# Kernel tuning notes

Hardware: AMD Instinct MI355X
Metric: run time of the kernel (lower is better)

The kernel has to match this reference:

```python
import jax, jax.numpy as jnp
import numpy as np

D = 100  # input_size


def _gru_scan(x, h0, wi, wh, bi, bh):
    # x: [B,T,Din], h0: [B,H], wi: [3H,Din], wh: [3H,H]  (PyTorch r,z,n gate order)
    xw = jnp.einsum('btd,gd->btg', x, wi) + bi  # [B,T,3H]
    def step(h, xt):
        gh = h @ wh.T + bh
        xr, xz, xn = jnp.split(xt, 3, axis=-1)
        hr, hz, hn = jnp.split(gh, 3, axis=-1)
        r = jax.nn.sigmoid(xr + hr)
        z = jax.nn.sigmoid(xz + hz)
        n = jnp.tanh(xn + r * hn)
        hn2 = (1 - z) * n + z * h
        return hn2, hn2
    _, ys = jax.lax.scan(step, h0, jnp.swapaxes(xw, 0, 1))
    return jnp.swapaxes(ys, 0, 1)  # [B,T,H]


def _bigru(x, wi, wh, bi, bh):
    B = x.shape[0]
    H = wh.shape[-1]
    h0 = jnp.zeros((B, H), x.dtype)
    f = _gru_scan(x, h0, wi[0], wh[0], bi[0], bh[0])
    b = _gru_scan(x[:, ::-1], h0, wi[1], wh[1], bi[1], bh[1])[:, ::-1]
    return jnp.concatenate([f, b], axis=-1)


def _gru_cell(x, h, wi, wh, bi, bh):
    gx = x @ wi.T + bi
    gh = h @ wh.T + bh
    xr, xz, xn = jnp.split(gx, 3, axis=-1)
    hr, hz, hn = jnp.split(gh, 3, axis=-1)
    r = jax.nn.sigmoid(xr + hr)
    z = jax.nn.sigmoid(xz + hz)
    n = jnp.tanh(xn + r * hn)
    return (1 - z) * n + z * h


def setup_inputs() -> dict:
    key = jax.random.key(0)
    ks = iter(jax.random.split(key, 40))
    def n(shape, s=0.08):
        return (jax.random.normal(next(ks), shape) * s).astype(jnp.float32)
    B, T, L, V = 32, 512, 64, 400000
    inp = {
        'x_word': jax.random.randint(next(ks), (B, T), 0, V),
        'x_query': jax.random.randint(next(ks), (B, L), 0, V),
        'embed': n((V, D), 0.3),
        'ctx_wi': n((2, 3 * D, D)), 'ctx_wh': n((2, 3 * D, D)),
        'ctx_bi': n((2, 3 * D)), 'ctx_bh': n((2, 3 * D)),
        'mod0_wi': n((2, 3 * D, 8 * D)), 'mod0_wh': n((2, 3 * D, D)),
        'mod0_bi': n((2, 3 * D)), 'mod0_bh': n((2, 3 * D)),
        'mod1_wi': n((2, 3 * D, 2 * D)), 'mod1_wh': n((2, 3 * D, D)),
        'mod1_bi': n((2, 3 * D)), 'mod1_bh': n((2, 3 * D)),
        'w_sim': n((6 * D,)),
        'enc_wi': n((12 * D, 2 * D)), 'enc_wh': n((12 * D, 4 * D)),
        'enc_bi': n((12 * D,)), 'enc_bh': n((12 * D,)),
        'dec_wi': n((12 * D, 2 * D)), 'dec_wh': n((12 * D, 4 * D)),
        'dec_bi': n((12 * D,)), 'dec_bh': n((12 * D,)),
        'w1': n((2 * D, 4 * D)), 'w2': n((2 * D, 4 * D)), 'vt': n((2 * D,)),
    }
    return inp


def reference(x_word, x_query, embed, ctx_wi, ctx_wh, ctx_bi, ctx_bh,
              mod0_wi, mod0_wh, mod0_bi, mod0_bh, mod1_wi, mod1_wh, mod1_bi, mod1_bh,
              w_sim, enc_wi, enc_wh, enc_bi, enc_bh, dec_wi, dec_wh, dec_bi, dec_bh,
              w1, w2, vt):
    B, T = x_word.shape
    # shared bidirectional context encoder over both context and query
    h = _bigru(embed[x_word], ctx_wi, ctx_wh, ctx_bi, ctx_bh)   # [B,T,2D]
    u = _bigru(embed[x_query], ctx_wi, ctx_wh, ctx_bi, ctx_bh)  # [B,L,2D]
    # trilinear similarity W @ cat(h,u,h*u), fused (no [B,T,L,6D] materialization)
    w1s, w2s, w3s = jnp.split(w_sim, 3)
    S = (jnp.einsum('btd,d->bt', h, w1s)[:, :, None]
         + jnp.einsum('bld,d->bl', u, w2s)[:, None, :]
         + jnp.einsum('btd,bld->btl', h * w3s, u))               # [B,T,L]
    c2q = jnp.einsum('btl,bld->btd', jax.nn.softmax(S, axis=-1), u)
    b_att = jax.nn.softmax(jnp.max(S, axis=2), axis=-1)          # [B,T]
    q2c = jnp.einsum('bt,btd->bd', b_att, h)[:, None, :]         # [B,1,2D]
    G = jnp.concatenate([h, c2q, h * c2q, h * q2c], axis=-1)     # [B,T,8D]
    # 2-layer bidirectional modeling GRU
    M = _bigru(G, mod0_wi, mod0_wh, mod0_bi, mod0_bh)
    M = _bigru(M, mod1_wi, mod1_wh, mod1_bi, mod1_bh)            # [B,T,2D]
    # pointer network
    enc = _gru_scan(M, jnp.zeros((B, 4 * D), M.dtype), enc_wi, enc_wh, enc_bi, enc_bh)  # [B,T,4D]
    enc_w1 = jnp.einsum('bth,ph->btp', enc, w1)                  # precompute W1 @ enc
    hid = jnp.zeros((B, 4 * D), M.dtype)
    dec_in = jnp.zeros((B, 2 * D), M.dtype)  # never updated (as in original)
    probs = []
    for _ in range(2):  # answers = 2 (start, end)
        hid = _gru_cell(dec_in, hid, dec_wi, dec_wh, dec_bi, dec_bh)
        blend = jnp.tanh(enc_w1 + (hid @ w2.T)[:, None, :])      # [B,T,2D]
        out = jnp.einsum('btp,p->bt', blend, vt)
        probs.append(jax.nn.log_softmax(out, axis=-1))
    return jnp.stack(probs, axis=1)  # [B,2,T]
```

## Files before the change

kernel.cpp:

```cpp
#include <hip/hip_runtime.h>
#include <hip/hip_bf16.h>

typedef __hip_bfloat16 bf16;
typedef unsigned long long u64;
typedef __attribute__((ext_vector_type(8))) short s8v;
typedef __attribute__((ext_vector_type(4))) short s4v;
typedef __attribute__((ext_vector_type(4))) float f4v;

#define DEV __device__ __forceinline__

DEV float to_f32(float x) { return x; }
DEV float to_f32(bf16 x) { return __bfloat162float(x); }
DEV void store_c(float* p, float v) { *p = v; }
DEV void store_c(bf16* p, float v) { *p = __float2bfloat16(v); }
DEV float sigmf(float x) { return 1.f / (1.f + __expf(-x)); }

__global__ void gather_embed_bf(const int* __restrict__ idx, const float* __restrict__ embed,
                                bf16* __restrict__ out, int ntok) {
  int i = blockIdx.x * blockDim.x + threadIdx.x;
  if (i >= ntok * 100) return;
  int t = i / 100;
  int d = i - t * 100;
  out[i] = __float2bfloat16(embed[(size_t)idx[t] * 100 + d]);
}

__global__ void cvt_bf16(const float* __restrict__ in, bf16* __restrict__ out, int n) {
  int i = blockIdx.x * blockDim.x + threadIdx.x;
  if (i < n) out[i] = __float2bfloat16(in[i]);
}

template <typename TC, bool HAS_BIAS>
__global__ __launch_bounds__(256) void gemm_mfma(
    const bf16* __restrict__ A, const bf16* __restrict__ W,
    const float* __restrict__ bias, TC* __restrict__ C,
    int M, int N, int K) {
  __shared__ short Als[128 * 32];
  __shared__ short Wls[64 * 32];
  const int tid = threadIdx.x;
  const int m0 = blockIdx.x * 128;
  const int n0 = blockIdx.y * 64;
  const int lane = tid & 63;
  const int wv = tid >> 6;
  const int wm = wv >> 1, wn = wv & 1;
  const int lq = lane >> 4, lr = lane & 15;
  const int arow = tid >> 1;
  const int ah = tid & 1;
  const int wrow = (tid & 127) >> 1;

  f4v acc[4][2];
#pragma unroll
  for (int i = 0; i < 4; ++i)
#pragma unroll
    for (int j = 0; j < 2; ++j) acc[i][j] = (f4v){0.f, 0.f, 0.f, 0.f};

  for (int k0 = 0; k0 < K; k0 += 32) {
#pragma unroll
    for (int ss = 0; ss < 2; ++ss) {
      int s = 2 * ah + ss;
      int kk = k0 + s * 8;
      short* dst = &Als[arow * 32 + s * 8];
      const short* src = (const short*)(A + (size_t)(m0 + arow) * K + kk);
      if (kk + 8 <= K) {
        *(s4v*)dst = *(const s4v*)src;
        *(s4v*)(dst + 4) = *(const s4v*)(src + 4);
      } else {
#pragma unroll
        for (int j = 0; j < 8; ++j) dst[j] = (kk + j < K) ? src[j] : (short)0;
      }
    }
    if (tid < 128) {
      int nrow = n0 + wrow;
#pragma unroll
      for (int ss = 0; ss < 2; ++ss) {
        int s = 2 * (tid & 1) + ss;
        int kk = k0 + s * 8;
        short* dst = &Wls[wrow * 32 + s * 8];
        if (nrow < N) {
          const short* src = (const short*)(W + (size_t)nrow * K + kk);
          if (kk + 8 <= K) {
            *(s4v*)dst = *(const s4v*)src;
            *(s4v*)(dst + 4) = *(const s4v*)(src + 4);
          } else {
#pragma unroll
            for (int j = 0; j < 8; ++j) dst[j] = (kk + j < K) ? src[j] : (short)0;
          }
        } else {
#pragma unroll
          for (int j = 0; j < 8; ++j) dst[j] = (short)0;
        }
      }
    }
    __syncthreads();
    s8v af[4], bfr[2];
#pragma unroll
    for (int mi = 0; mi < 4; ++mi) {
      int r = wm * 64 + mi * 16 + lr;
      af[mi] = *(const s8v*)&Als[r * 32 + lq * 8];
    }
#pragma unroll
    for (int ni = 0; ni < 2; ++ni) {
      int r = wn * 32 + ni * 16 + lr;
      bfr[ni] = *(const s8v*)&Wls[r * 32 + lq * 8];
    }
#pragma unroll
    for (int mi = 0; mi < 4; ++mi)
#pragma unroll
      for (int ni = 0; ni < 2; ++ni)
        acc[mi][ni] = __builtin_amdgcn_mfma_f32_16x16x32_bf16(af[mi], bfr[ni], acc[mi][ni], 0, 0, 0);
    __syncthreads();
  }
#pragma unroll
  for (int mi = 0; mi < 4; ++mi) {
#pragma unroll
    for (int ni = 0; ni < 2; ++ni) {
      int n = n0 + wn * 32 + ni * 16 + lr;
      if (n >= N) continue;
      float bv = HAS_BIAS ? bias[n] : 0.f;
#pragma unroll
      for (int r = 0; r < 4; ++r) {
        int m = m0 + wm * 64 + mi * 16 + lq * 4 + r;
        store_c(&C[(size_t)m * N + n], acc[mi][ni][r] + bv);
      }
    }
  }
}

template <typename TO>
__global__ __launch_bounds__(320) void gru_scan100_reg(
    const bf16* __restrict__ xw_f, const bf16* __restrict__ xw_b,
    const float* __restrict__ wh,
    const float* __restrict__ bh,
    TO* __restrict__ out,
    int T) {
  const int b = blockIdx.x, dir = blockIdx.y;
  const bf16* xw = dir ? xw_b : xw_f;
  __shared__ float h_s[100];
  __shared__ float g_s[300];
  const int tid = threadIdx.x;
  float w[100];
  float bias = 0.f;
  if (tid < 300) {
    const float* wrow = wh + (size_t)dir * 30000 + (size_t)tid * 100;
#pragma unroll
    for (int c = 0; c < 25; ++c) {
      float4 v = *(const float4*)(wrow + 4 * c);
      w[4 * c] = v.x; w[4 * c + 1] = v.y; w[4 * c + 2] = v.z; w[4 * c + 3] = v.w;
    }
    bias = bh[dir * 300 + tid];
  }
  if (tid < 100) h_s[tid] = 0.f;
  __syncthreads();
  for (int step = 0; step < T; ++step) {
    int t = dir ? (T - 1 - step) : step;
    if (tid < 300) {
      float a0 = bias, a1 = 0.f, a2 = 0.f, a3 = 0.f;
#pragma unroll
      for (int c = 0; c < 25; ++c) {
        float4 h4 = *(const float4*)(&h_s[4 * c]);
        a0 += w[4 * c] * h4.x; a1 += w[4 * c + 1] * h4.y;
        a2 += w[4 * c + 2] * h4.z; a3 += w[4 * c + 3] * h4.w;
      }
      g_s[tid] = (a0 + a1) + (a2 + a3);
    }
    __syncthreads();
    if (tid < 100) {
      size_t base = ((size_t)b * T + t) * 300;
      float xr = to_f32(xw[base + tid]);
      float xz = to_f32(xw[base + 100 + tid]);
      float xn = to_f32(xw[base + 200 + tid]);
      float rr = sigmf(xr + g_s[tid]);
      float zz = sigmf(xz + g_s[100 + tid]);
      float nn = tanhf(xn + rr * g_s[200 + tid]);
      float hn = (1.f - zz) * nn + zz * h_s[tid];
      h_s[tid] = hn;
      store_c(&out[((size_t)b * T + t) * 200 + dir * 100 + tid], hn);
    }
    __syncthreads();
  }
}

__global__ __launch_bounds__(640) void gru_scan_enc_tag(
    const bf16* __restrict__ xw,
    const float* __restrict__ wh,
    const float* __restrict__ bh,
    bf16* __restrict__ out,
    u64* __restrict__ hx,
    int T) {
  const int b = blockIdx.x, s = blockIdx.y;
  __shared__ float h_s[400];
  __shared__ float g_s[150];
  const int tid = threadIdx.x;
  const int g = tid >> 2, p = tid & 3;
  const bool active = (tid < 600);
  float w[100];
  float bias = 0.f;
  if (active) {
    int i = g % 50, grp = g / 50;
    int gidx = grp * 400 + s * 50 + i;
    const float* wrow = wh + (size_t)gidx * 400 + p * 100;
#pragma unroll
    for (int c = 0; c < 25; ++c) {
      float4 v = *(const float4*)(wrow + 4 * c);
      w[4 * c] = v.x; w[4 * c + 1] = v.y; w[4 * c + 2] = v.z; w[4 * c + 3] = v.w;
    }
    if (p == 0) bias = bh[gidx];
  }
  for (int k = tid; k < 400; k += 640) h_s[k] = 0.f;
  const int myi = s * 50 + tid;
  float pxr = 0.f, pxz = 0.f, pxn = 0.f;
  if (tid < 50) {
    size_t base0 = (size_t)b * T * 1200;
    pxr = to_f32(xw[base0 + myi]);
    pxz = to_f32(xw[base0 + 400 + myi]);
    pxn = to_f32(xw[base0 + 800 + myi]);
  }
  __syncthreads();

  for (int t = 0; t < T; ++t) {
    if (active) {
      float a0 = bias, a1 = 0.f, a2 = 0.f, a3 = 0.f;
      const int hb = p * 100;
#pragma unroll
      for (int c = 0; c < 25; ++c) {
        float4 h4 = *(const float4*)(&h_s[hb + 4 * c]);
        a0 += w[4 * c] * h4.x; a1 += w[4 * c + 1] * h4.y;
        a2 += w[4 * c + 2] * h4.z; a3 += w[4 * c + 3] * h4.w;
      }
      float acc = (a0 + a1) + (a2 + a3);
      acc += __shfl_xor(acc, 1);
      acc += __shfl_xor(acc, 2);
      if (p == 0) g_s[g] = acc;
    }
    __syncthreads();
    const int par = (t + 1) & 1;
    u64* hxp = hx + ((size_t)b * 2 + par) * 400;
    if (tid < 50) {
      float rr = sigmf(pxr + g_s[tid]);
      float zz = sigmf(pxz + g_s[50 + tid]);
      float nn = tanhf(pxn + rr * g_s[100 + tid]);
      float hn = (1.f - zz) * nn + zz * h_s[myi];
      out[((size_t)b * T + t) * 400 + myi] = __float2bfloat16(hn);
      h_s[myi] = hn;
      u64 pack = (u64)__float_as_uint(hn) | ((u64)(unsigned)(t + 1) << 32);
      __hip_atomic_store(&hxp[myi], pack, __ATOMIC_RELAXED, __HIP_MEMORY_SCOPE_AGENT);
      if (t + 1 < T) {
        size_t basen = ((size_t)b * T + (t + 1)) * 1200;
        pxr = to_f32(xw[basen + myi]);
        pxz = to_f32(xw[basen + 400 + myi]);
        pxn = to_f32(xw[basen + 800 + myi]);
      }
    }
    if (tid < 400 && (tid / 50) != s) {
      const u64* src = &hxp[tid];
      u64 v;
      for (;;) {
        v = __hip_atomic_load(src, __ATOMIC_RELAXED, __HIP_MEMORY_SCOPE_AGENT);
        if ((unsigned)(v >> 32) == (unsigned)(t + 1)) break;
        __builtin_amdgcn_s_sleep(1);
      }
      h_s[tid] = __uint_as_float((unsigned)v);
    }
    __syncthreads();
  }
}

__global__ __launch_bounds__(64) void rowdot200(const float* __restrict__ X, const float* __restrict__ w,
                                                float* __restrict__ out, int rows) {
  int r = blockIdx.x;
  int lane = threadIdx.x;
  const float* x = X + (size_t)r * 200;
  float s = x[lane] * w[lane] + x[lane + 64] * w[lane + 64] + x[lane + 128] * w[lane + 128];
  if (lane < 8) s += x[lane + 192] * w[lane + 192];
  for (int off = 32; off; off >>= 1) s += __shfl_down(s, off);
  if (lane == 0) out[r] = s;
}

__global__ __launch_bounds__(256) void attn_main(
    const float* __restrict__ h,
    const float* __restrict__ u,
    const float* __restrict__ th,
    const float* __restrict__ tu,
    const float* __restrict__ w_sim,
    float* __restrict__ c2q,
    float* __restrict__ smax,
    int T) {
  const int b = blockIdx.x;
  const int t0 = blockIdx.y * 32;
  __shared__ float u_s[64 * 201];
  __shared__ float tu_s[64];
  __shared__ float w3_s[200];
  __shared__ float hw3_s[200];
  __shared__ float Sp[4][64];
  __shared__ float A_s[64];
  const int tid = threadIdx.x;
  for (int i = tid; i < 64 * 200; i += 256) {
    int l = i / 200, d = i - l * 200;
    u_s[l * 201 + d] = u[((size_t)b * 64 + l) * 200 + d];
  }
  if (tid < 64) tu_s[tid] = tu[b * 64 + tid];
  if (tid < 200) w3_s[tid] = w_sim[400 + tid];
  __syncthreads();
  for (int tt = 0; tt < 32; ++tt) {
    int t = t0 + tt;
    if (tid < 200) hw3_s[tid] = h[((size_t)b * T + t) * 200 + tid] * w3_s[tid];
    __syncthreads();
    int l = tid & 63, q = tid >> 6;
    float p = 0.f;
    for (int d = q * 50; d < q * 50 + 50; ++d) p += hw3_s[d] * u_s[l * 201 + d];
    Sp[q][l] = p;
    __syncthreads();
    if (tid < 64) {
      float s = th[b * T + t] + tu_s[l] + Sp[0][l] + Sp[1][l] + Sp[2][l] + Sp[3][l];
      float m = s;
      for (int off = 32; off; off >>= 1) m = fmaxf(m, __shfl_xor(m, off));
      float e = __expf(s - m);
      float ssum = e;
      for (int off = 32; off; off >>= 1) ssum += __shfl_xor(ssum, off);
      A_s[l] = e / ssum;
      if (l == 0) smax[b * T + t] = m;
    }
    __syncthreads();
    if (tid < 200) {
      float acc = 0.f;
      for (int l2 = 0; l2 < 64; ++l2) acc += A_s[l2] * u_s[l2 * 201 + tid];
      c2q[((size_t)b * T + t) * 200 + tid] = acc;
    }
    __syncthreads();
  }
}

__global__ __launch_bounds__(256) void softmax_T(const float* __restrict__ in, float* __restrict__ outv, int T) {
  int b = blockIdx.x;
  int tid = threadIdx.x;
  __shared__ float red[256];
  float m = -1e30f;
  for (int t = tid; t < T; t += 256) m = fmaxf(m, in[b * T + t]);
  red[tid] = m;
  __syncthreads();
  for (int s = 128; s; s >>= 1) {
    if (tid < s) red[tid] = fmaxf(red[tid], red[tid + s]);
    __syncthreads();
  }
  m = red[0];
  __syncthreads();
  float sum = 0.f;
  for (int t = tid; t < T; t += 256) sum += __expf(in[b * T + t] - m);
  red[tid] = sum;
  __syncthreads();
  for (int s = 128; s; s >>= 1) {
    if (tid < s) red[tid] += red[tid + s];
    __syncthreads();
  }
  float inv = 1.f / red[0];
  for (int t = tid; t < T; t += 256) outv[b * T + t] = __expf(in[b * T + t] - m) * inv;
}

__global__ __launch_bounds__(256) void q2c_kernel(const float* __restrict__ batt, const float* __restrict__ h,
                                                  float* __restrict__ q2c, int T) {
  int b = blockIdx.x;
  int tid = threadIdx.x;
  if (tid < 200) {
    float acc = 0.f;
    for (int t = 0; t < T; ++t) acc += batt[b * T + t] * h[((size_t)b * T + t) * 200 + tid];
    q2c[b * 200 + tid] = acc;
  }
}

__global__ void build_G(const float* __restrict__ h, const float* __restrict__ c2q,
                        const float* __restrict__ q2c, bf16* __restrict__ G, int T) {
  size_t i = (size_t)blockIdx.x * blockDim.x + threadIdx.x;
  if (i >= (size_t)32 * T * 200) return;
  size_t row = i / 200;
  int d = (int)(i - row * 200);
  int b = (int)(row / T);
  float hv = h[i];
  float cv = c2q[i];
  float qv = q2c[b * 200 + d];
  bf16* g = G + row * 800;
  g[d] = __float2bfloat16(hv);
  g[200 + d] = __float2bfloat16(cv);
  g[400 + d] = __float2bfloat16(hv * cv);
  g[600 + d] = __float2bfloat16(hv * qv);
}

__global__ __launch_bounds__(512) void decoder_small(
    const float* __restrict__ dwh,
    const float* __restrict__ dbi, const float* __restrict__ dbh,
    const float* __restrict__ w2,
    float* __restrict__ d2out) {
  __shared__ float hid[400];
  __shared__ float hid2[400];
  __shared__ float gh[1200];
  const int tid = threadIdx.x;
  if (tid < 400) {
    float r = sigmf(dbi[tid] + dbh[tid]);
    float z = sigmf(dbi[400 + tid] + dbh[400 + tid]);
    float n = tanhf(dbi[800 + tid] + r * dbh[800 + tid]);
    hid[tid] = (1.f - z) * n;
  }
  __syncthreads();
  if (tid < 200) {
    float a = 0.f;
    for (int k = 0; k < 400; ++k) a += w2[(size_t)tid * 400 + k] * hid[k];
    d2out[tid] = a;
  }
  for (int j = tid; j < 1200; j += 512) {
    float a = dbh[j];
    for (int k = 0; k < 400; ++k) a += dwh[(size_t)j * 400 + k] * hid[k];
    gh[j] = a;
  }
  __syncthreads();
  if (tid < 400) {
    float r = sigmf(dbi[tid] + gh[tid]);
    float z = sigmf(dbi[400 + tid] + gh[400 + tid]);
    float n = tanhf(dbi[800 + tid] + r * gh[800 + tid]);
    hid2[tid] = (1.f - z) * n + z * hid[tid];
  }
  __syncthreads();
  if (tid < 200) {
    float a = 0.f;
    for (int k = 0; k < 400; ++k) a += w2[(size_t)tid * 400 + k] * hid2[k];
    d2out[200 + tid] = a;
  }
}

__global__ __launch_bounds__(64) void logits_kernel(
    const float* __restrict__ encw1,
    const float* __restrict__ d2,
    const float* __restrict__ vt,
    float* __restrict__ outp,
    int T) {
  int row = blockIdx.x;
  int b = row / T, t = row - b * T;
  int lane = threadIdx.x;
  const float* e = encw1 + (size_t)row * 200;
  float s0 = 0.f, s1 = 0.f;
  for (int p = lane; p < 200; p += 64) {
    float ev = e[p], v = vt[p];
    s0 += tanhf(ev + d2[p]) * v;
    s1 += tanhf(ev + d2[200 + p]) * v;
  }
  for (int off = 32; off; off >>= 1) {
    s0 += __shfl_down(s0, off);
    s1 += __shfl_down(s1, off);
  }
  if (lane == 0) {
    outp[((size_t)b * 2 + 0) * T + t] = s0;
    outp[((size_t)b * 2 + 1) * T + t] = s1;
  }
}

__global__ __launch_bounds__(256) void log_softmax_T(float* __restrict__ x, int T) {
  int row = blockIdx.x;
  float* p = x + (size_t)row * T;
  __shared__ float red[256];
  int tid = threadIdx.x;
  float m = -1e30f;
  for (int t = tid; t < T; t += 256) m = fmaxf(m, p[t]);
  red[tid] = m;
  __syncthreads();
  for (int s = 128; s; s >>= 1) {
    if (tid < s) red[tid] = fmaxf(red[tid], red[tid + s]);
    __syncthreads();
  }
  m = red[0];
  __syncthreads();
  float sum = 0.f;
  for (int t = tid; t < T; t += 256) sum += __expf(p[t] - m);
  red[tid] = sum;
  __syncthreads();
  for (int s = 128; s; s >>= 1) {
    if (tid < s) red[tid] += red[tid + s];
    __syncthreads();
  }
  float lse = m + __logf(red[0]);
  __syncthreads();
  for (int t = tid; t < T; t += 256) p[t] = p[t] - lse;
}

extern "C" void kernel_launch(void* const* d_in, const int* in_sizes, int n_in,
                              void* d_out, int out_size, void* d_ws, size_t ws_size,
                              hipStream_t stream) {
  (void)in_sizes; (void)n_in; (void)out_size; (void)ws_size;
  const int B = 32, T = 512, L = 64;
  const int BT = B * T;
  const int BL = B * L;

  const int* x_word = (const int*)d_in[0];
  const int* x_query = (const int*)d_in[1];
  const float* embed = (const float*)d_in[2];
  const float* ctx_wi = (const float*)d_in[3];
  const float* ctx_wh = (const float*)d_in[4];
  const float* ctx_bi = (const float*)d_in[5];
  const float* ctx_bh = (const float*)d_in[6];
  const float* mod0_wi = (const float*)d_in[7];
  const float* mod0_wh = (const float*)d_in[8];
  const float* mod0_bi = (const float*)d_in[9];
  const float* mod0_bh = (const float*)d_in[10];
  const float* mod1_wi = (const float*)d_in[11];
  const float* mod1_wh = (const float*)d_in[12];
  const float* mod1_bi = (const float*)d_in[13];
  const float* mod1_bh = (const float*)d_in[14];
  const float* w_sim = (const float*)d_in[15];
  const float* enc_wi = (const float*)d_in[16];
  const float* enc_wh = (const float*)d_in[17];
  const float* enc_bi = (const float*)d_in[18];
  const float* enc_bh = (const float*)d_in[19];
  const float* dec_wh = (const float*)d_in[21];
  const float* dec_bi = (const float*)d_in[22];
  const float* dec_bh = (const float*)d_in[23];
  const float* w1 = (const float*)d_in[24];
  const float* w2 = (const float*)d_in[25];
  const float* vt = (const float*)d_in[26];
  float* out_f = (float*)d_out;

  char* ws = (char*)d_ws;
  size_t off = 0;
  auto alloc = [&](size_t bytes) -> void* {
    void* p = ws + off;
    off += (bytes + 255) & ~(size_t)255;
    return p;
  };
  u64* hx = (u64*)alloc((size_t)B * 2 * 400 * 8);
  bf16* ewbf = (bf16*)alloc((size_t)BT * 100 * 2);
  bf16* eqbf = (bf16*)alloc((size_t)BL * 100 * 2);
  bf16* ctx_wibf = (bf16*)alloc((size_t)60000 * 2);
  bf16* mod0_wibf = (bf16*)alloc((size_t)480000 * 2);
  bf16* mod1_wibf = (bf16*)alloc((size_t)120000 * 2);
  bf16* enc_wibf = (bf16*)alloc((size_t)240000 * 2);
  bf16* w1bf = (bf16*)alloc((size_t)80000 * 2);
  char* RA = (char*)alloc((size_t)BT * 1200 * 2);
  bf16* xwA = (bf16*)RA;
  bf16* xwB = (bf16*)(RA + (size_t)BT * 300 * 2);
  bf16* xwe = (bf16*)RA;
  bf16* xwqF = (bf16*)alloc((size_t)BL * 300 * 2);
  bf16* xwqB = (bf16*)alloc((size_t)BL * 300 * 2);
  char* RB = (char*)alloc((size_t)BT * 800 * 2);
  bf16* G = (bf16*)RB;
  bf16* enc_outbf = (bf16*)RB;
  char* RC = (char*)alloc((size_t)2 * BT * 200 * 4);
  float* h_cat = (float*)RC;
  float* c2q = (float*)(RC + (size_t)BT * 200 * 4);
  bf16* M0bf = (bf16*)c2q;
  bf16* Mxbf = (bf16*)h_cat;
  float* encw1 = c2q;
  float* u_cat = (float*)alloc((size_t)BL * 200 * 4);
  float* th = (float*)alloc((size_t)BT * 4);
  float* tu = (float*)alloc((size_t)BL * 4);
  float* smaxb = (float*)alloc((size_t)BT * 4);
  float* batt = (float*)alloc((size_t)BT * 4);
  float* q2cb = (float*)alloc((size_t)B * 200 * 4);
  float* d2 = (float*)alloc((size_t)400 * 4);

  hipMemsetAsync(hx, 0, (size_t)B * 2 * 400 * 8, stream);

  cvt_bf16<<<(60000 + 255) / 256, 256, 0, stream>>>(ctx_wi, ctx_wibf, 60000);
  cvt_bf16<<<(480000 + 255) / 256, 256, 0, stream>>>(mod0_wi, mod0_wibf, 480000);
  cvt_bf16<<<(120000 + 255) / 256, 256, 0, stream>>>(mod1_wi, mod1_wibf, 120000);
  cvt_bf16<<<(240000 + 255) / 256, 256, 0, stream>>>(enc_wi, enc_wibf, 240000);
  cvt_bf16<<<(80000 + 255) / 256, 256, 0, stream>>>(w1, w1bf, 80000);
  gather_embed_bf<<<(BT * 100 + 255) / 256, 256, 0, stream>>>(x_word, embed, ewbf, BT);
  gather_embed_bf<<<(BL * 100 + 255) / 256, 256, 0, stream>>>(x_query, embed, eqbf, BL);

  {
    dim3 g(BT / 128, (300 + 63) / 64);
    gemm_mfma<bf16, true><<<g, 256, 0, stream>>>(ewbf, ctx_wibf, ctx_bi, xwA, BT, 300, 100);
    gemm_mfma<bf16, true><<<g, 256, 0, stream>>>(ewbf, ctx_wibf + 30000, ctx_bi + 300, xwB, BT, 300, 100);
    dim3 gq(BL / 128, (300 + 63) / 64);
    gemm_mfma<bf16, true><<<gq, 256, 0, stream>>>(eqbf, ctx_wibf, ctx_bi, xwqF, BL, 300, 100);
    gemm_mfma<bf16, true><<<gq, 256, 0, stream>>>(eqbf, ctx_wibf + 30000, ctx_bi + 300, xwqB, BL, 300, 100);
  }

  gru_scan100_reg<float><<<dim3(B, 2), 320, 0, stream>>>(xwA, xwB, ctx_wh, ctx_bh, h_cat, T);
  gru_scan100_reg<float><<<dim3(B, 2), 320, 0, stream>>>(xwqF, xwqB, ctx_wh, ctx_bh, u_cat, L);

  rowdot200<<<BT, 64, 0, stream>>>(h_cat, w_sim, th, BT);
  rowdot200<<<BL, 64, 0, stream>>>(u_cat, w_sim + 200, tu, BL);
  attn_main<<<dim3(B, T / 32), 256, 0, stream>>>(h_cat, u_cat, th, tu, w_sim, c2q, smaxb, T);
  softmax_T<<<B, 256, 0, stream>>>(smaxb, batt, T);
  q2c_kernel<<<B, 256, 0, stream>>>(batt, h_cat, q2cb, T);
  build_G<<<(BT * 200 + 255) / 256, 256, 0, stream>>>(h_cat, c2q, q2cb, G, T);

  {
    dim3 g(BT / 128, (300 + 63) / 64);
    gemm_mfma<bf16, true><<<g, 256, 0, stream>>>(G, mod0_wibf, mod0_bi, xwA, BT, 300, 800);
    gemm_mfma<bf16, true><<<g, 256, 0, stream>>>(G, mod0_wibf + 240000, mod0_bi + 300, xwB, BT, 300, 800);
  }
  gru_scan100_reg<bf16><<<dim3(B, 2), 320, 0, stream>>>(xwA, xwB, mod0_wh, mod0_bh, M0bf, T);

  {
    dim3 g(BT / 128, (300 + 63) / 64);
    gemm_mfma<bf16, true><<<g, 256, 0, stream>>>(M0bf, mod1_wibf, mod1_bi, xwA, BT, 300, 200);
    gemm_mfma<bf16, true><<<g, 256, 0, stream>>>(M0bf, mod1_wibf + 60000, mod1_bi + 300, xwB, BT, 300, 200);
  }
  gru_scan100_reg<bf16><<<dim3(B, 2), 320, 0, stream>>>(xwA, xwB, mod1_wh, mod1_bh, Mxbf, T);

  {
    dim3 g(BT / 128, (1200 + 63) / 64);
    gemm_mfma<bf16, true><<<g, 256, 0, stream>>>(Mxbf, enc_wibf, enc_bi, xwe, BT, 1200, 200);
  }
  gru_scan_enc_tag<<<dim3(B, 8), 640, 0, stream>>>(xwe, enc_wh, enc_bh, enc_outbf, hx, T);
  {
    dim3 g(BT / 128, (200 + 63) / 64);
    gemm_mfma<float, false><<<g, 256, 0, stream>>>(enc_outbf, w1bf, nullptr, encw1, BT, 200, 400);
  }

  decoder_small<<<1, 512, 0, stream>>>(dec_wh, dec_bi, dec_bh, w2, d2);
  logits_kernel<<<BT, 64, 0, stream>>>(encw1, d2, vt, out_f, T);
  log_softmax_T<<<B * 2, 256, 0, stream>>>(out_f, T);
}
```

Measured before the change: 3.580 ms.

## Process two batch rows per encoder GRU block and prefetch gate inputs

The encoder GRU scan now handles two batch elements per block, reusing the register-resident recurrent weights for both hidden states. This halves the number of blocks and cross-block spin-waits while doubling work per step, so weight loads and sync overhead are amortized. Separately, the 100-wide bidirectional scan now prefetches the next timestep's input-gate values into registers during the current step, taking the global load latency off the serial critical path. The trade-off is a longer per-step critical path in the encoder, since each step runs two matvecs and two spin-waits in sequence, and fewer blocks to spread across the CUs.

```diff
diff --git a/kernel.cpp b/kernel.cpp
--- a/kernel.cpp
+++ b/kernel.cpp
@@ -149,6 +149,14 @@
     bias = bh[dir * 300 + tid];
   }
   if (tid < 100) h_s[tid] = 0.f;
+  float pxr = 0.f, pxz = 0.f, pxn = 0.f;
+  if (tid < 100) {
+    int t0 = dir ? (T - 1) : 0;
+    size_t base = ((size_t)b * T + t0) * 300;
+    pxr = to_f32(xw[base + tid]);
+    pxz = to_f32(xw[base + 100 + tid]);
+    pxn = to_f32(xw[base + 200 + tid]);
+  }
   __syncthreads();
   for (int step = 0; step < T; ++step) {
     int t = dir ? (T - 1 - step) : step;
@@ -164,31 +172,35 @@
     }
     __syncthreads();
     if (tid < 100) {
-      size_t base = ((size_t)b * T + t) * 300;
-      float xr = to_f32(xw[base + tid]);
-      float xz = to_f32(xw[base + 100 + tid]);
-      float xn = to_f32(xw[base + 200 + tid]);
-      float rr = sigmf(xr + g_s[tid]);
-      float zz = sigmf(xz + g_s[100 + tid]);
-      float nn = tanhf(xn + rr * g_s[200 + tid]);
+      float rr = sigmf(pxr + g_s[tid]);
+      float zz = sigmf(pxz + g_s[100 + tid]);
+      float nn = tanhf(pxn + rr * g_s[200 + tid]);
       float hn = (1.f - zz) * nn + zz * h_s[tid];
       h_s[tid] = hn;
       store_c(&out[((size_t)b * T + t) * 200 + dir * 100 + tid], hn);
-    }
-    __syncthreads();
-  }
-}
-
-__global__ __launch_bounds__(640) void gru_scan_enc_tag(
+      if (step + 1 < T) {
+        int tn = dir ? (T - 2 - step) : (step + 1);
+        size_t basen = ((size_t)b * T + tn) * 300;
+        pxr = to_f32(xw[basen + tid]);
+        pxz = to_f32(xw[basen + 100 + tid]);
+        pxn = to_f32(xw[basen + 200 + tid]);
+      }
+    }
+    __syncthreads();
+  }
+}
+
+__global__ __launch_bounds__(640) void gru_scan_enc_tag2(
     const bf16* __restrict__ xw,
     const float* __restrict__ wh,
     const float* __restrict__ bh,
     bf16* __restrict__ out,
     u64* __restrict__ hx,
     int T) {
-  const int b = blockIdx.x, s = blockIdx.y;
-  __shared__ float h_s[400];
-  __shared__ float g_s[150];
+  const int pair = blockIdx.x, s = blockIdx.y;
+  const int bA = 2 * pair, bB = 2 * pair + 1;
+  __shared__ float hA[400], hB[400];
+  __shared__ float gA[150], gB[150];
   const int tid = threadIdx.x;
   const int g = tid >> 2, p = tid & 3;
   const bool active = (tid < 600);
@@ -205,60 +217,95 @@
     }
     if (p == 0) bias = bh[gidx];
   }
-  for (int k = tid; k < 400; k += 640) h_s[k] = 0.f;
+  for (int k = tid; k < 400; k += 640) { hA[k] = 0.f; hB[k] = 0.f; }
   const int myi = s * 50 + tid;
-  float pxr = 0.f, pxz = 0.f, pxn = 0.f;
+  float pxrA = 0.f, pxzA = 0.f, pxnA = 0.f;
+  float pxrB = 0.f, pxzB = 0.f, pxnB = 0.f;
   if (tid < 50) {
-    size_t base0 = (size_t)b * T * 1200;
-    pxr = to_f32(xw[base0 + myi]);
-    pxz = to_f32(xw[base0 + 400 + myi]);
-    pxn = to_f32(xw[base0 + 800 + myi]);
+    size_t baseA = (size_t)bA * T * 1200, baseB = (size_t)bB * T * 1200;
+    pxrA = to_f32(xw[baseA + myi]);
+    pxzA = to_f32(xw[baseA + 400 + myi]);
+    pxnA = to_f32(xw[baseA + 800 + myi]);
+    pxrB = to_f32(xw[baseB + myi]);
+    pxzB = to_f32(xw[baseB + 400 + myi]);
+    pxnB = to_f32(xw[baseB + 800 + myi]);
   }
   __syncthreads();
 
   for (int t = 0; t < T; ++t) {
     if (active) {
+      const int hb = p * 100;
       float a0 = bias, a1 = 0.f, a2 = 0.f, a3 = 0.f;
-      const int hb = p * 100;
 #pragma unroll
       for (int c = 0; c < 25; ++c) {
-        float4 h4 = *(const float4*)(&h_s[hb + 4 * c]);
+        float4 h4 = *(const float4*)(&hA[hb + 4 * c]);
         a0 += w[4 * c] * h4.x; a1 += w[4 * c + 1] * h4.y;
         a2 += w[4 * c + 2] * h4.z; a3 += w[4 * c + 3] * h4.w;
       }
-      float acc = (a0 + a1) + (a2 + a3);
-      acc += __shfl_xor(acc, 1);
-      acc += __shfl_xor(acc, 2);
-      if (p == 0) g_s[g] = acc;
+      float accA = (a0 + a1) + (a2 + a3);
+      accA += __shfl_xor(accA, 1);
+      accA += __shfl_xor(accA, 2);
+      if (p == 0) gA[g] = accA;
+      float b0 = bias, b1 = 0.f, b2 = 0.f, b3 = 0.f;
+#pragma unroll
+      for (int c = 0; c < 25; ++c) {
+        float4 h4 = *(const float4*)(&hB[hb + 4 * c]);
+        b0 += w[4 * c] * h4.x; b1 += w[4 * c + 1] * h4.y;
+        b2 += w[4 * c + 2] * h4.z; b3 += w[4 * c + 3] * h4.w;
+      }
+      float accB = (b0 + b1) + (b2 + b3);
+      accB += __shfl_xor(accB, 1);
+      accB += __shfl_xor(accB, 2);
+      if (p == 0) gB[g] = accB;
     }
     __syncthreads();
     const int par = (t + 1) & 1;
-    u64* hxp = hx + ((size_t)b * 2 + par) * 400;
+    u64* hxA = hx + ((size_t)bA * 2 + par) * 400;
+    u64* hxB = hx + ((size_t)bB * 2 + par) * 400;
     if (tid < 50) {
-      float rr = sigmf(pxr + g_s[tid]);
-      float zz = sigmf(pxz + g_s[50 + tid]);
-      float nn = tanhf(pxn + rr * g_s[100 + tid]);
-      float hn = (1.f - zz) * nn + zz * h_s[myi];
-      out[((size_t)b * T + t) * 400 + myi] = __float2bfloat16(hn);
-      h_s[myi] = hn;
-      u64 pack = (u64)__float_as_uint(hn) | ((u64)(unsigned)(t + 1) << 32);
-      __hip_atomic_store(&hxp[myi], pack, __ATOMIC_RELAXED, __HIP_MEMORY_SCOPE_AGENT);
+      float rr = sigmf(pxrA + gA[tid]);
+      float zz = sigmf(pxzA + gA[50 + tid]);
+      float nn = tanhf(pxnA + rr * gA[100 + tid]);
+      float hnA = (1.f - zz) * nn + zz * hA[myi];
+      out[((size_t)bA * T + t) * 400 + myi] = __float2bfloat16(hnA);
+      hA[myi] = hnA;
+      u64 packA = (u64)__float_as_uint(hnA) | ((u64)(unsigned)(t + 1) << 32);
+      __hip_atomic_store(&hxA[myi], packA, __ATOMIC_RELAXED, __HIP_MEMORY_SCOPE_AGENT);
+      float rb = sigmf(pxrB + gB[tid]);
+      float zb = sigmf(pxzB + gB[50 + tid]);
+      float nb = tanhf(pxnB + rb * gB[100 + tid]);
+      float hnB = (1.f - zb) * nb + zb * hB[myi];
+      out[((size_t)bB * T + t) * 400 + myi] = __float2bfloat16(hnB);
+      hB[myi] = hnB;
+      u64 packB = (u64)__float_as_uint(hnB) | ((u64)(unsigned)(t + 1) << 32);
+      __hip_atomic_store(&hxB[myi], packB, __ATOMIC_RELAXED, __HIP_MEMORY_SCOPE_AGENT);
       if (t + 1 < T) {
-        size_t basen = ((size_t)b * T + (t + 1)) * 1200;
-        pxr = to_f32(xw[basen + myi]);
-        pxz = to_f32(xw[basen + 400 + myi]);
-        pxn = to_f32(xw[basen + 800 + myi]);
+        size_t baseA = ((size_t)bA * T + (t + 1)) * 1200;
+        size_t baseB = ((size_t)bB * T + (t + 1)) * 1200;
+        pxrA = to_f32(xw[baseA + myi]);
+        pxzA = to_f32(xw[baseA + 400 + myi]);
+        pxnA = to_f32(xw[baseA + 800 + myi]);
+        pxrB = to_f32(xw[baseB + myi]);
+        pxzB = to_f32(xw[baseB + 400 + myi]);
+        pxnB = to_f32(xw[baseB + 800 + myi]);
       }
     }
     if (tid < 400 && (tid / 50) != s) {
-      const u64* src = &hxp[tid];
+      const u64* srcA = &hxA[tid];
       u64 v;
       for (;;) {
-        v = __hip_atomic_load(src, __ATOMIC_RELAXED, __HIP_MEMORY_SCOPE_AGENT);
+        v = __hip_atomic_load(srcA, __ATOMIC_RELAXED, __HIP_MEMORY_SCOPE_AGENT);
         if ((unsigned)(v >> 32) == (unsigned)(t + 1)) break;
         __builtin_amdgcn_s_sleep(1);
       }
-      h_s[tid] = __uint_as_float((unsigned)v);
+      hA[tid] = __uint_as_float((unsigned)v);
+      const u64* srcB = &hxB[tid];
+      for (;;) {
+        v = __hip_atomic_load(srcB, __ATOMIC_RELAXED, __HIP_MEMORY_SCOPE_AGENT);
+        if ((unsigned)(v >> 32) == (unsigned)(t + 1)) break;
+        __builtin_amdgcn_s_sleep(1);
+      }
+      hB[tid] = __uint_as_float((unsigned)v);
     }
     __syncthreads();
   }
@@ -276,14 +323,10 @@
 }
 
 __global__ __launch_bounds__(256) void attn_main(
-    const float* __restrict__ h,
-    const float* __restrict__ u,
-    const float* __restrict__ th,
-    const float* __restrict__ tu,
-    const float* __restrict__ w_sim,
-    float* __restrict__ c2q,
-    float* __restrict__ smax,
-    int T) {
+    const float* __restrict__ h, const float* __restrict__ u,
+    const float* __restrict__ th, const float* __restrict__ tu,
+    const float* __restrict__ w_sim, float* __restrict__ c2q,
+    float* __restrict__ smax, int T) {
   const int b = blockIdx.x;
   const int t0 = blockIdx.y * 32;
   __shared__ float u_s[64 * 201];
@@ -384,9 +427,8 @@
 }
 
 __global__ __launch_bounds__(512) void decoder_small(
-    const float* __restrict__ dwh,
-    const float* __restrict__ dbi, const float* __restrict__ dbh,
-    const float* __restrict__ w2,
+    const float* __restrict__ dwh, const float* __restrict__ dbi,
+    const float* __restrict__ dbh, const float* __restrict__ w2,
     float* __restrict__ d2out) {
   __shared__ float hid[400];
   __shared__ float hid2[400];
@@ -425,11 +467,8 @@
 }
 
 __global__ __launch_bounds__(64) void logits_kernel(
-    const float* __restrict__ encw1,
-    const float* __restrict__ d2,
-    const float* __restrict__ vt,
-    float* __restrict__ outp,
-    int T) {
+    const float* __restrict__ encw1, const float* __restrict__ d2,
+    const float* __restrict__ vt, float* __restrict__ outp, int T) {
   int row = blockIdx.x;
   int b = row / T, t = row - b * T;
   int lane = threadIdx.x;
@@ -599,7 +638,7 @@
     dim3 g(BT / 128, (1200 + 63) / 64);
     gemm_mfma<bf16, true><<<g, 256, 0, stream>>>(Mxbf, enc_wibf, enc_bi, xwe, BT, 1200, 200);
   }
-  gru_scan_enc_tag<<<dim3(B, 8), 640, 0, stream>>>(xwe, enc_wh, enc_bh, enc_outbf, hx, T);
+  gru_scan_enc_tag2<<<dim3(B / 2, 8), 640, 0, stream>>>(xwe, enc_wh, enc_bh, enc_outbf, hx, T);
   {
     dim3 g(BT / 128, (200 + 63) / 64);
     gemm_mfma<float, false><<<g, 256, 0, stream>>>(enc_outbf, w1bf, nullptr, encw1, BT, 200, 400);
```

Measured after the change: 3.894 ms. 8.8% more time.

## Compute two gate rows per thread in GRU scans and prefetch next-step inputs

Applied to the files above, without the earlier changes.

Each active thread in both recurrent scan kernels now holds two weight rows (200 registers of weights) and computes two gate dot products per step, sharing each h_s load between them. This shrinks the blocks from 320 to 192 threads and from 640 to 448 threads, so fewer waves take part in every step's barrier and each shared-memory load of the hidden state feeds twice as many FMAs. The 100-unit scan also loads the next timestep's input projections one step early, moving the global load latency off the serial path. The costs are much higher register pressure, with a risk of spills or lower occupancy, and less parallel FMA throughput per step.

```diff
diff --git a/kernel.cpp b/kernel.cpp
--- a/kernel.cpp
+++ b/kernel.cpp
@@ -126,7 +126,7 @@
 }
 
 template <typename TO>
-__global__ __launch_bounds__(320) void gru_scan100_reg(
+__global__ __launch_bounds__(192) void gru_scan100_reg(
     const bf16* __restrict__ xw_f, const bf16* __restrict__ xw_b,
     const float* __restrict__ wh,
     const float* __restrict__ bh,
@@ -137,49 +137,67 @@
   __shared__ float h_s[100];
   __shared__ float g_s[300];
   const int tid = threadIdx.x;
-  float w[100];
-  float bias = 0.f;
-  if (tid < 300) {
-    const float* wrow = wh + (size_t)dir * 30000 + (size_t)tid * 100;
+  float w0[100], w1[100];
+  float bias0 = 0.f, bias1 = 0.f;
+  if (tid < 150) {
+    const float* wr0 = wh + (size_t)dir * 30000 + (size_t)(2 * tid) * 100;
 #pragma unroll
     for (int c = 0; c < 25; ++c) {
-      float4 v = *(const float4*)(wrow + 4 * c);
-      w[4 * c] = v.x; w[4 * c + 1] = v.y; w[4 * c + 2] = v.z; w[4 * c + 3] = v.w;
-    }
-    bias = bh[dir * 300 + tid];
+      float4 v = *(const float4*)(wr0 + 4 * c);
+      w0[4 * c] = v.x; w0[4 * c + 1] = v.y; w0[4 * c + 2] = v.z; w0[4 * c + 3] = v.w;
+      float4 u = *(const float4*)(wr0 + 100 + 4 * c);
+      w1[4 * c] = u.x; w1[4 * c + 1] = u.y; w1[4 * c + 2] = u.z; w1[4 * c + 3] = u.w;
+    }
+    bias0 = bh[dir * 300 + 2 * tid];
+    bias1 = bh[dir * 300 + 2 * tid + 1];
   }
   if (tid < 100) h_s[tid] = 0.f;
+  float pxr = 0.f, pxz = 0.f, pxn = 0.f;
+  if (tid < 100) {
+    int t0 = dir ? (T - 1) : 0;
+    size_t base = ((size_t)b * T + t0) * 300;
+    pxr = to_f32(xw[base + tid]);
+    pxz = to_f32(xw[base + 100 + tid]);
+    pxn = to_f32(xw[base + 200 + tid]);
+  }
   __syncthreads();
   for (int step = 0; step < T; ++step) {
     int t = dir ? (T - 1 - step) : step;
-    if (tid < 300) {
-      float a0 = bias, a1 = 0.f, a2 = 0.f, a3 = 0.f;
+    if (tid < 150) {
+      float a0 = bias0, a1 = 0.f, a2 = 0.f, a3 = 0.f;
+      float b0 = bias1, b1 = 0.f, b2 = 0.f, b3 = 0.f;
 #pragma unroll
       for (int c = 0; c < 25; ++c) {
         float4 h4 = *(const float4*)(&h_s[4 * c]);
-        a0 += w[4 * c] * h4.x; a1 += w[4 * c + 1] * h4.y;
-        a2 += w[4 * c + 2] * h4.z; a3 += w[4 * c + 3] * h4.w;
-      }
-      g_s[tid] = (a0 + a1) + (a2 + a3);
+        a0 += w0[4 * c] * h4.x; a1 += w0[4 * c + 1] * h4.y;
+        a2 += w0[4 * c + 2] * h4.z; a3 += w0[4 * c + 3] * h4.w;
+        b0 += w1[4 * c] * h4.x; b1 += w1[4 * c + 1] * h4.y;
+        b2 += w1[4 * c + 2] * h4.z; b3 += w1[4 * c + 3] * h4.w;
+      }
+      g_s[2 * tid] = (a0 + a1) + (a2 + a3);
+      g_s[2 * tid + 1] = (b0 + b1) + (b2 + b3);
     }
     __syncthreads();
     if (tid < 100) {
-      size_t base = ((size_t)b * T + t) * 300;
-      float xr = to_f32(xw[base + tid]);
-      float xz = to_f32(xw[base + 100 + tid]);
-      float xn = to_f32(xw[base + 200 + tid]);
-      float rr = sigmf(xr + g_s[tid]);
-      float zz = sigmf(xz + g_s[100 + tid]);
-      float nn = tanhf(xn + rr * g_s[200 + tid]);
+      float rr = sigmf(pxr + g_s[tid]);
+      float zz = sigmf(pxz + g_s[100 + tid]);
+      float nn = tanhf(pxn + rr * g_s[200 + tid]);
       float hn = (1.f - zz) * nn + zz * h_s[tid];
       h_s[tid] = hn;
       store_c(&out[((size_t)b * T + t) * 200 + dir * 100 + tid], hn);
-    }
-    __syncthreads();
-  }
-}
-
-__global__ __launch_bounds__(640) void gru_scan_enc_tag(
+      if (step + 1 < T) {
+        int tn = dir ? (T - 2 - step) : (step + 1);
+        size_t basen = ((size_t)b * T + tn) * 300;
+        pxr = to_f32(xw[basen + tid]);
+        pxz = to_f32(xw[basen + 100 + tid]);
+        pxn = to_f32(xw[basen + 200 + tid]);
+      }
+    }
+    __syncthreads();
+  }
+}
+
+__global__ __launch_bounds__(448) void gru_scan_enc_tag(
     const bf16* __restrict__ xw,
     const float* __restrict__ wh,
     const float* __restrict__ bh,
@@ -190,22 +208,28 @@
   __shared__ float h_s[400];
   __shared__ float g_s[150];
   const int tid = threadIdx.x;
-  const int g = tid >> 2, p = tid & 3;
-  const bool active = (tid < 600);
-  float w[100];
-  float bias = 0.f;
+  const int q = tid >> 2, p = tid & 3;
+  const bool active = (tid < 300);
+  float w0[100], w1[100];
+  float bias0 = 0.f, bias1 = 0.f;
   if (active) {
-    int i = g % 50, grp = g / 50;
-    int gidx = grp * 400 + s * 50 + i;
-    const float* wrow = wh + (size_t)gidx * 400 + p * 100;
+    int g0 = 2 * q, g1 = 2 * q + 1;
+    int i0 = g0 % 50, grp0 = g0 / 50;
+    int i1 = g1 % 50, grp1 = g1 / 50;
+    int row0 = grp0 * 400 + s * 50 + i0;
+    int row1 = grp1 * 400 + s * 50 + i1;
+    const float* wr0 = wh + (size_t)row0 * 400 + p * 100;
+    const float* wr1 = wh + (size_t)row1 * 400 + p * 100;
 #pragma unroll
     for (int c = 0; c < 25; ++c) {
-      float4 v = *(const float4*)(wrow + 4 * c);
-      w[4 * c] = v.x; w[4 * c + 1] = v.y; w[4 * c + 2] = v.z; w[4 * c + 3] = v.w;
-    }
-    if (p == 0) bias = bh[gidx];
-  }
-  for (int k = tid; k < 400; k += 640) h_s[k] = 0.f;
+      float4 v = *(const float4*)(wr0 + 4 * c);
+      w0[4 * c] = v.x; w0[4 * c + 1] = v.y; w0[4 * c + 2] = v.z; w0[4 * c + 3] = v.w;
+      float4 u = *(const float4*)(wr1 + 4 * c);
+      w1[4 * c] = u.x; w1[4 * c + 1] = u.y; w1[4 * c + 2] = u.z; w1[4 * c + 3] = u.w;
+    }
+    if (p == 0) { bias0 = bh[row0]; bias1 = bh[row1]; }
+  }
+  for (int k = tid; k < 400; k += 448) h_s[k] = 0.f;
   const int myi = s * 50 + tid;
   float pxr = 0.f, pxz = 0.f, pxn = 0.f;
   if (tid < 50) {
@@ -218,18 +242,24 @@
 
   for (int t = 0; t < T; ++t) {
     if (active) {
-      float a0 = bias, a1 = 0.f, a2 = 0.f, a3 = 0.f;
       const int hb = p * 100;
+      float a0 = bias0, a1 = 0.f, a2 = 0.f, a3 = 0.f;
+      float b0 = bias1, b1 = 0.f, b2 = 0.f, b3 = 0.f;
 #pragma unroll
       for (int c = 0; c < 25; ++c) {
         float4 h4 = *(const float4*)(&h_s[hb + 4 * c]);
-        a0 += w[4 * c] * h4.x; a1 += w[4 * c + 1] * h4.y;
-        a2 += w[4 * c + 2] * h4.z; a3 += w[4 * c + 3] * h4.w;
-      }
-      float acc = (a0 + a1) + (a2 + a3);
-      acc += __shfl_xor(acc, 1);
-      acc += __shfl_xor(acc, 2);
-      if (p == 0) g_s[g] = acc;
+        a0 += w0[4 * c] * h4.x; a1 += w0[4 * c + 1] * h4.y;
+        a2 += w0[4 * c + 2] * h4.z; a3 += w0[4 * c + 3] * h4.w;
+        b0 += w1[4 * c] * h4.x; b1 += w1[4 * c + 1] * h4.y;
+        b2 += w1[4 * c + 2] * h4.z; b3 += w1[4 * c + 3] * h4.w;
+      }
+      float acc0 = (a0 + a1) + (a2 + a3);
+      float acc1 = (b0 + b1) + (b2 + b3);
+      acc0 += __shfl_xor(acc0, 1);
+      acc0 += __shfl_xor(acc0, 2);
+      acc1 += __shfl_xor(acc1, 1);
+      acc1 += __shfl_xor(acc1, 2);
+      if (p == 0) { g_s[2 * q] = acc0; g_s[2 * q + 1] = acc1; }
     }
     __syncthreads();
     const int par = (t + 1) & 1;
@@ -276,14 +306,10 @@
 }
 
 __global__ __launch_bounds__(256) void attn_main(
-    const float* __restrict__ h,
-    const float* __restrict__ u,
-    const float* __restrict__ th,
-    const float* __restrict__ tu,
-    const float* __restrict__ w_sim,
-    float* __restrict__ c2q,
-    float* __restrict__ smax,
-    int T) {
+    const float* __restrict__ h, const float* __restrict__ u,
+    const float* __restrict__ th, const float* __restrict__ tu,
+    const float* __restrict__ w_sim, float* __restrict__ c2q,
+    float* __restrict__ smax, int T) {
   const int b = blockIdx.x;
   const int t0 = blockIdx.y * 32;
   __shared__ float u_s[64 * 201];
@@ -384,9 +410,8 @@
 }
 
 __global__ __launch_bounds__(512) void decoder_small(
-    const float* __restrict__ dwh,
-    const float* __restrict__ dbi, const float* __restrict__ dbh,
-    const float* __restrict__ w2,
+    const float* __restrict__ dwh, const float* __restrict__ dbi,
+    const float* __restrict__ dbh, const float* __restrict__ w2,
     float* __restrict__ d2out) {
   __shared__ float hid[400];
   __shared__ float hid2[400];
@@ -425,11 +450,8 @@
 }
 
 __global__ __launch_bounds__(64) void logits_kernel(
-    const float* __restrict__ encw1,
-    const float* __restrict__ d2,
-    const float* __restrict__ vt,
-    float* __restrict__ outp,
-    int T) {
+    const float* __restrict__ encw1, const float* __restrict__ d2,
+    const float* __restrict__ vt, float* __restrict__ outp, int T) {
   int row = blockIdx.x;
   int b = row / T, t = row - b * T;
   int lane = threadIdx.x;
@@ -571,8 +593,8 @@
     gemm_mfma<bf16, true><<<gq, 256, 0, stream>>>(eqbf, ctx_wibf + 30000, ctx_bi + 300, xwqB, BL, 300, 100);
   }
 
-  gru_scan100_reg<float><<<dim3(B, 2), 320, 0, stream>>>(xwA, xwB, ctx_wh, ctx_bh, h_cat, T);
-  gru_scan100_reg<float><<<dim3(B, 2), 320, 0, stream>>>(xwqF, xwqB, ctx_wh, ctx_bh, u_cat, L);
+  gru_scan100_reg<float><<<dim3(B, 2), 192, 0, stream>>>(xwA, xwB, ctx_wh, ctx_bh, h_cat, T);
+  gru_scan100_reg<float><<<dim3(B, 2), 192, 0, stream>>>(xwqF, xwqB, ctx_wh, ctx_bh, u_cat, L);
 
   rowdot200<<<BT, 64, 0, stream>>>(h_cat, w_sim, th, BT);
   rowdot200<<<BL, 64, 0, stream>>>(u_cat, w_sim + 200, tu, BL);
@@ -586,20 +608,20 @@
     gemm_mfma<bf16, true><<<g, 256, 0, stream>>>(G, mod0_wibf, mod0_bi, xwA, BT, 300, 800);
     gemm_mfma<bf16, true><<<g, 256, 0, stream>>>(G, mod0_wibf + 240000, mod0_bi + 300, xwB, BT, 300, 800);
   }
-  gru_scan100_reg<bf16><<<dim3(B, 2), 320, 0, stream>>>(xwA, xwB, mod0_wh, mod0_bh, M0bf, T);
+  gru_scan100_reg<bf16><<<dim3(B, 2), 192, 0, stream>>>(xwA, xwB, mod0_wh, mod0_bh, M0bf, T);
 
   {
     dim3 g(BT / 128, (300 + 63) / 64);
     gemm_mfma<bf16, true><<<g, 256, 0, stream>>>(M0bf, mod1_wibf, mod1_bi, xwA, BT, 300, 200);
     gemm_mfma<bf16, true><<<g, 256, 0, stream>>>(M0bf, mod1_wibf + 60000, mod1_bi + 300, xwB, BT, 300, 200);
   }
-  gru_scan100_reg<bf16><<<dim3(B, 2), 320, 0, stream>>>(xwA, xwB, mod1_wh, mod1_bh, Mxbf, T);
+  gru_scan100_reg<bf16><<<dim3(B, 2), 192, 0, stream>>>(xwA, xwB, mod1_wh, mod1_bh, Mxbf, T);
 
   {
     dim3 g(BT / 128, (1200 + 63) / 64);
     gemm_mfma<bf16, true><<<g, 256, 0, stream>>>(Mxbf, enc_wibf, enc_bi, xwe, BT, 1200, 200);
   }
-  gru_scan_enc_tag<<<dim3(B, 8), 640, 0, stream>>>(xwe, enc_wh, enc_bh, enc_outbf, hx, T);
+  gru_scan_enc_tag<<<dim3(B, 8), 448, 0, stream>>>(xwe, enc_wh, enc_bh, enc_outbf, hx, T);
   {
     dim3 g(BT / 128, (200 + 63) / 64);
     gemm_mfma<float, false><<<g, 256, 0, stream>>>(enc_outbf, w1bf, nullptr, encw1, BT, 200, 400);
```

Result: faster. 3.299 ms (-7.9%).
